# Optimization experiments

Measured on AMD Instinct MI355X. Metric: run time of the kernel, lower is better.

## Reference

```python
import jax, jax.numpy as jnp
import numpy as np

B, T_ENC, T_OUT = 64, 1024, 1000
N_MELS, ENC_D, DEC_H, ATTN_D = 80, 256, 256, 256


def setup_inputs() -> dict:
    key = jax.random.key(0)
    ks = jax.random.split(key, 24)

    def p(k, shape, scale=0.05):
        return jax.random.normal(k, shape, dtype=jnp.float32) * scale

    lengths = jax.random.randint(ks[0], (B,), T_ENC // 2, T_ENC + 1)
    enc_mask = (jnp.arange(T_ENC)[None, :] < lengths[:, None]).astype(jnp.float32)
    return {
        "enc_outputs": jax.random.normal(ks[1], (B, T_ENC, ENC_D), dtype=jnp.float32),
        "target_mel": jax.random.normal(ks[2], (B, T_OUT, N_MELS), dtype=jnp.float32),
        # attention params
        "W_enc": p(ks[3], (ATTN_D, ENC_D)), "b_enc": jnp.zeros((ATTN_D,), jnp.float32),
        "W_dec": p(ks[4], (ATTN_D, DEC_H)), "b_dec": jnp.zeros((ATTN_D,), jnp.float32),
        "v_w": p(ks[5], (1, ATTN_D)), "v_b": jnp.zeros((1,), jnp.float32),
        # prenet
        "pre_W1": p(ks[6], (DEC_H, N_MELS)), "pre_b1": jnp.zeros((DEC_H,), jnp.float32),
        "pre_W2": p(ks[7], (DEC_H, DEC_H)), "pre_b2": jnp.zeros((DEC_H,), jnp.float32),
        # LSTMCell (PyTorch gate order i, f, g, o)
        "W_ih": p(ks[8], (4 * DEC_H, DEC_H + ENC_D)), "W_hh": p(ks[9], (4 * DEC_H, DEC_H)),
        "b_ih": jnp.zeros((4 * DEC_H,), jnp.float32), "b_hh": jnp.zeros((4 * DEC_H,), jnp.float32),
        # output heads
        "mel_W": p(ks[10], (N_MELS, DEC_H + ENC_D)), "mel_b": jnp.zeros((N_MELS,), jnp.float32),
        "stop_W": p(ks[11], (1, DEC_H + ENC_D)), "stop_b": jnp.zeros((1,), jnp.float32),
        "enc_mask": enc_mask,
    }


def reference(enc_outputs, target_mel, W_enc, b_enc, W_dec, b_dec, v_w, v_b,
              pre_W1, pre_b1, pre_W2, pre_b2, W_ih, W_hh, b_ih, b_hh,
              mel_W, mel_b, stop_W, stop_b, enc_mask):
    Bsz = enc_outputs.shape[0]
    H = W_hh.shape[1]
    NEG = jnp.float32(-1e9)
    # precompute encoder projection once, as the original does
    attn_enc = jnp.einsum('bte,ae->bta', enc_outputs, W_enc) + b_enc  # (B, T_enc, A)
    # teacher forcing: input at step t is target_mel[t-1], zeros at t=0
    prev_inputs = jnp.concatenate(
        [jnp.zeros_like(target_mel[:, :1]), target_mel[:, :-1]], axis=1)
    xs = jnp.swapaxes(prev_inputs, 0, 1)  # (T_out, B, n_mels)

    def step(carry, prev):
        h, c = carry
        attn_dec = h @ W_dec.T + b_dec                                  # (B, A)
        energy = jnp.tanh(attn_enc + attn_dec[:, None, :]) @ v_w[0] + v_b[0]  # (B, T_enc)
        energy = jnp.where(enc_mask == 0, NEG, energy)
        attn = jax.nn.softmax(energy, axis=-1)
        context = jnp.einsum('bt,btd->bd', attn, enc_outputs)           # (B, enc_d)
        pre = jax.nn.relu(prev @ pre_W1.T + pre_b1)                     # dropout = identity (eval)
        pre = jax.nn.relu(pre @ pre_W2.T + pre_b2)
        x = jnp.concatenate([pre, context], axis=1)
        gates = x @ W_ih.T + b_ih + h @ W_hh.T + b_hh                   # (B, 4H)
        i, f, g, o = jnp.split(gates, 4, axis=1)
        c_new = jax.nn.sigmoid(f) * c + jax.nn.sigmoid(i) * jnp.tanh(g)
        h_new = jax.nn.sigmoid(o) * jnp.tanh(c_new)
        comb = jnp.concatenate([h_new, context], axis=1)
        mel = comb @ mel_W.T + mel_b
        stop = (comb @ stop_W.T + stop_b)[:, 0]
        return (h_new, c_new), (mel, stop)

    h0 = jnp.zeros((Bsz, H), dtype=enc_outputs.dtype)
    _, (mels, stops) = jax.lax.scan(step, (h0, h0), xs)
    return jnp.swapaxes(mels, 0, 1), jnp.swapaxes(stops, 0, 1)
```

## Files before the change

kernel.cpp:

```cpp
#include <hip/hip_runtime.h>
#include <hip/hip_bf16.h>

#define NMEL 80

__device__ __forceinline__ float bf2f(unsigned short u) {
  unsigned v = ((unsigned)u) << 16; float f; __builtin_memcpy(&f, &v, 4); return f;
}
__device__ __forceinline__ unsigned short f2bf_u(float f) {
  __hip_bfloat16 h = __float2bfloat16(f); unsigned short u; __builtin_memcpy(&u, &h, 2); return u;
}
__device__ __forceinline__ float agload(const float* p) {
  return __hip_atomic_load(p, __ATOMIC_RELAXED, __HIP_MEMORY_SCOPE_AGENT);
}
__device__ __forceinline__ void agstore(float* p, float v) {
  __hip_atomic_store(p, v, __ATOMIC_RELAXED, __HIP_MEMORY_SCOPE_AGENT);
}

constexpr size_t OFF_ATTNT = 0;
constexpr size_t SZ_ATTNT = (size_t)64 * 256 * 1024 * 4;
constexpr size_t OFF_PRE2 = OFF_ATTNT + SZ_ATTNT;
constexpr size_t SZ_PRE2 = (size_t)64000 * 256 * 2;
constexpr size_t OFF_WIC4 = OFF_PRE2 + SZ_PRE2;
constexpr size_t SZ_W4 = (size_t)4 * 64 * 256 * 4 * 4;
constexpr size_t OFF_WPRE4 = OFF_WIC4 + SZ_W4;
constexpr size_t OFF_WHH4 = OFF_WPRE4 + SZ_W4;
constexpr size_t OFF_WDECT = OFF_WHH4 + SZ_W4;
constexpr size_t SZ_WDECT = (size_t)4 * 64 * 256 * 4;
constexpr size_t OFF_MELT = OFF_WDECT + SZ_WDECT;
constexpr size_t SZ_MELT = (size_t)4 * 128 * 80 * 4;
constexpr size_t OFF_STOPT = OFF_MELT + SZ_MELT;
constexpr size_t SZ_STOPT = (size_t)4 * 128 * 4;
constexpr size_t OFF_BIASG = OFF_STOPT + SZ_STOPT;
constexpr size_t SZ_BIASG = (size_t)4 * 256 * 4;
constexpr size_t OFF_EXCH = (OFF_BIASG + SZ_BIASG + 255) & ~(size_t)255;
constexpr size_t EXF_DEC = 0;
constexpr size_t EXN_DEC = (size_t)2 * 64 * 4 * 256;
constexpr size_t EXF_GH = EXF_DEC + EXN_DEC;
constexpr size_t EXN_GH = (size_t)2 * 64 * 4 * 1024;
constexpr size_t EXF_CTX = EXF_GH + EXN_GH;
constexpr size_t EXN_CTX = (size_t)64 * 4 * 256;
constexpr size_t EXF_S = EXF_CTX + EXN_CTX;
constexpr size_t EXN_S = 64 * 16;
constexpr size_t EXF_CTR = EXF_S + EXN_S;
constexpr size_t EXN_CTR = 64 * 16;
constexpr size_t EXCH_FLOATS = EXF_CTR + EXN_CTR;
constexpr size_t SZ_EXCH = EXCH_FLOATS * 4;
constexpr size_t WS_NEED = OFF_EXCH + SZ_EXCH;

__global__ __launch_bounds__(256) void prep_weights(
    const float* __restrict__ W_ih, const float* __restrict__ W_hh,
    const float* __restrict__ W_dec, const float* __restrict__ mel_W,
    const float* __restrict__ stop_W, const float* __restrict__ b_ih,
    const float* __restrict__ b_hh,
    float* __restrict__ Wic4, float* __restrict__ Wpre4, float* __restrict__ Whh4,
    float* __restrict__ WdecT, float* __restrict__ MelT, float* __restrict__ StopT,
    float* __restrict__ biasG) {
  int idx = blockIdx.x * 256 + threadIdx.x;
  if (idx < 262144) {
    int q = idx & 3, j = (idx >> 2) & 255, c4 = (idx >> 10) & 63, s = idx >> 16;
    int row = (j >> 6) * 256 + s * 64 + (j & 63);
    Wic4[idx] = W_ih[(size_t)row * 512 + 256 + c4 * 4 + q];
    Wpre4[idx] = W_ih[(size_t)row * 512 + c4 * 4 + q];
    Whh4[idx] = W_hh[(size_t)(j * 4 + q) * 256 + s * 64 + c4];
  } else if (idx < 262144 + 65536) {
    int k = idx - 262144;
    int a = k & 255, hh = (k >> 8) & 63, s = k >> 14;
    WdecT[k] = W_dec[(size_t)a * 256 + s * 64 + hh];
  } else if (idx < 262144 + 65536 + 40960) {
    int k = idx - (262144 + 65536);
    int m = k % 80, r = k / 80;
    int cc = r & 127, s = r >> 7;
    int col = (cc < 64) ? (s * 64 + cc) : (256 + s * 64 + (cc - 64));
    MelT[k] = mel_W[(size_t)m * 512 + col];
  } else if (idx < 262144 + 65536 + 40960 + 512) {
    int k = idx - (262144 + 65536 + 40960);
    int cc = k & 127, s = k >> 7;
    int col = (cc < 64) ? (s * 64 + cc) : (256 + s * 64 + (cc - 64));
    StopT[k] = stop_W[col];
  } else if (idx < 262144 + 65536 + 40960 + 512 + 1024) {
    int k = idx - (262144 + 65536 + 40960 + 512);
    int j = k & 255, s = k >> 8;
    int row = (j >> 6) * 256 + s * 64 + (j & 63);
    biasG[k] = b_ih[row] + b_hh[row];
  }
}

__global__ __launch_bounds__(256) void attn_gemm(const float* __restrict__ enc,
                                                 const float* __restrict__ W_enc,
                                                 const float* __restrict__ b_enc,
                                                 float* __restrict__ attnT) {
  __shared__ unsigned short Alds[64 * 260];
  const int tid = threadIdx.x;
  const int row0 = blockIdx.x * 64;
  const int wv = tid >> 6, lane = tid & 63, nb = wv * 64;
  for (int idx = tid; idx < 64 * 256; idx += 256) {
    int r = idx >> 8, k = idx & 255;
    Alds[r * 260 + k] = f2bf_u(enc[(size_t)(row0 + r) * 256 + k]);
  }
  __syncthreads();
  float acc[64];
#pragma unroll
  for (int n = 0; n < 64; ++n) acc[n] = b_enc[nb + n];
  for (int k8 = 0; k8 < 256; k8 += 8) {
    ushort4 ua = *(const ushort4*)&Alds[lane * 260 + k8];
    ushort4 ub = *(const ushort4*)&Alds[lane * 260 + k8 + 4];
    float a0 = bf2f(ua.x), a1 = bf2f(ua.y), a2 = bf2f(ua.z), a3 = bf2f(ua.w);
    float a4 = bf2f(ub.x), a5 = bf2f(ub.y), a6 = bf2f(ub.z), a7 = bf2f(ub.w);
#pragma unroll
    for (int n = 0; n < 64; ++n) {
      const float4* wp = (const float4*)(W_enc + (size_t)(nb + n) * 256 + k8);
      float4 w0 = wp[0], w1 = wp[1];
      acc[n] = fmaf(a0, w0.x, acc[n]); acc[n] = fmaf(a1, w0.y, acc[n]);
      acc[n] = fmaf(a2, w0.z, acc[n]); acc[n] = fmaf(a3, w0.w, acc[n]);
      acc[n] = fmaf(a4, w1.x, acc[n]); acc[n] = fmaf(a5, w1.y, acc[n]);
      acc[n] = fmaf(a6, w1.z, acc[n]); acc[n] = fmaf(a7, w1.w, acc[n]);
    }
  }
  const float CE = 2.8853900817779268f;
  const int b = row0 >> 10;
  const int te = (row0 & 1023) + lane;
#pragma unroll
  for (int n = 0; n < 64; ++n) {
    int a = nb + n;
    attnT[(((size_t)b) << 18) + (((size_t)(a >> 2)) << 12) + (((size_t)te) << 2) + (a & 3)] =
        acc[n] * CE;
  }
}

__global__ __launch_bounds__(256) void prenet_fused(const float* __restrict__ tmel,
                                                    const float* __restrict__ W1,
                                                    const float* __restrict__ b1,
                                                    const float* __restrict__ W2,
                                                    const float* __restrict__ b2,
                                                    unsigned short* __restrict__ pre2) {
  __shared__ unsigned short Alds[64 * 260];
  const int tid = threadIdx.x;
  const int row0 = blockIdx.x * 64;
  const int wv = tid >> 6, lane = tid & 63, nb = wv * 64;
  for (int idx = tid; idx < 64 * 80; idx += 256) {
    int r = idx / 80, k = idx - r * 80;
    int R = row0 + r;
    float v = (R % 1000 != 0) ? tmel[(size_t)(R - 1) * NMEL + k] : 0.f;
    Alds[r * 260 + k] = f2bf_u(v);
  }
  __syncthreads();
  float acc[64];
#pragma unroll
  for (int n = 0; n < 64; ++n) acc[n] = b1[nb + n];
  for (int k8 = 0; k8 < 80; k8 += 8) {
    ushort4 ua = *(const ushort4*)&Alds[lane * 260 + k8];
    ushort4 ub = *(const ushort4*)&Alds[lane * 260 + k8 + 4];
    float a0 = bf2f(ua.x), a1 = bf2f(ua.y), a2 = bf2f(ua.z), a3 = bf2f(ua.w);
    float a4 = bf2f(ub.x), a5 = bf2f(ub.y), a6 = bf2f(ub.z), a7 = bf2f(ub.w);
#pragma unroll
    for (int n = 0; n < 64; ++n) {
      const float4* wp = (const float4*)(W1 + (size_t)(nb + n) * 80 + k8);
      float4 w0 = wp[0], w1 = wp[1];
      acc[n] = fmaf(a0, w0.x, acc[n]); acc[n] = fmaf(a1, w0.y, acc[n]);
      acc[n] = fmaf(a2, w0.z, acc[n]); acc[n] = fmaf(a3, w0.w, acc[n]);
      acc[n] = fmaf(a4, w1.x, acc[n]); acc[n] = fmaf(a5, w1.y, acc[n]);
      acc[n] = fmaf(a6, w1.z, acc[n]); acc[n] = fmaf(a7, w1.w, acc[n]);
    }
  }
  __syncthreads();
#pragma unroll
  for (int n = 0; n < 64; ++n) Alds[lane * 260 + nb + n] = f2bf_u(fmaxf(acc[n], 0.f));
  __syncthreads();
#pragma unroll
  for (int n = 0; n < 64; ++n) acc[n] = b2[nb + n];
  for (int k8 = 0; k8 < 256; k8 += 8) {
    ushort4 ua = *(const ushort4*)&Alds[lane * 260 + k8];
    ushort4 ub = *(const ushort4*)&Alds[lane * 260 + k8 + 4];
    float a0 = bf2f(ua.x), a1 = bf2f(ua.y), a2 = bf2f(ua.z), a3 = bf2f(ua.w);
    float a4 = bf2f(ub.x), a5 = bf2f(ub.y), a6 = bf2f(ub.z), a7 = bf2f(ub.w);
#pragma unroll
    for (int n = 0; n < 64; ++n) {
      const float4* wp = (const float4*)(W2 + (size_t)(nb + n) * 256 + k8);
      float4 w0 = wp[0], w1 = wp[1];
      acc[n] = fmaf(a0, w0.x, acc[n]); acc[n] = fmaf(a1, w0.y, acc[n]);
      acc[n] = fmaf(a2, w0.z, acc[n]); acc[n] = fmaf(a3, w0.w, acc[n]);
      acc[n] = fmaf(a4, w1.x, acc[n]); acc[n] = fmaf(a5, w1.y, acc[n]);
      acc[n] = fmaf(a6, w1.z, acc[n]); acc[n] = fmaf(a7, w1.w, acc[n]);
    }
  }
  __syncthreads();
#pragma unroll
  for (int n = 0; n < 64; ++n) Alds[lane * 260 + nb + n] = f2bf_u(fmaxf(acc[n], 0.f));
  __syncthreads();
  for (int idx = tid; idx < 64 * 128; idx += 256) {
    int r = idx >> 7, k2 = (idx & 127) * 2;
    unsigned pair = (unsigned)Alds[r * 260 + k2] | ((unsigned)Alds[r * 260 + k2 + 1] << 16);
    *(unsigned*)(pre2 + (size_t)(row0 + r) * 256 + k2) = pair;
  }
}

__global__ __launch_bounds__(256) void decoder_loop(
    const float* __restrict__ attnT, const float* __restrict__ enc,
    const unsigned short* __restrict__ pre2,
    const float* __restrict__ Wic4, const float* __restrict__ Wpre4,
    const float* __restrict__ Whh4, const float* __restrict__ WdecT,
    const float* __restrict__ MelT, const float* __restrict__ StopT,
    const float* __restrict__ biasG,
    float* exch, unsigned* ctr,
    const float* __restrict__ b_dec, const float* __restrict__ v_w,
    const float* __restrict__ v_b, const float* __restrict__ enc_mask,
    const float* __restrict__ mel_b, const float* __restrict__ stop_b,
    float* out) {
  __shared__ float dec_lds[256], v2_lds[256], p_lds[256], ctx_lds[256], gates_lds[256];
  __shared__ float pre_lds[256];
  __shared__ float ctxp_lds[1024];
  __shared__ float c_lds[64], h_lds[64];
  __shared__ float red_lds[8];
  __shared__ float stop_lds[128];
  __shared__ float sv_lds;

  const int tid = threadIdx.x;
  const int wg = blockIdx.x;
  const int b = wg & 63, s = wg >> 6;
  const int lane = tid & 63, wid = tid >> 6;
  const float CE = 2.8853900817779268f;
  const float L2E = 1.4426950408889634f;

  if (tid < 64) c_lds[tid] = 0.f;
  v2_lds[tid] = -2.f * v_w[tid];
  {
    float sp = v_w[tid];
    for (int m = 32; m; m >>= 1) sp += __shfl_xor(sp, m);
    if (lane == 0) red_lds[wid] = sp;
  }
  __syncthreads();
  if (tid == 0) sv_lds = red_lds[0] + red_lds[1] + red_lds[2] + red_lds[3];
  __syncthreads();
  const float Sv = sv_lds;
  const float vb = v_b[0];
  const int te = s * 256 + tid;
  const float maskv = enc_mask[b * 1024 + te];
  const float bdec_r = b_dec[tid];
  const float biasg_r = biasG[s * 256 + tid];
  const float* attn_me4 = attnT + (((size_t)b) << 18) + (((size_t)te) << 2);
  const unsigned short* pre2_b = pre2 + (size_t)b * 1000 * 256;

  float* decP = exch + EXF_DEC;
  float* ghP = exch + EXF_GH;
  float* ctxP = exch + EXF_CTX;
  float* sP = exch + EXF_S;
  unsigned* ctrb = ctr + b * 16;
  unsigned epoch = 0;

  for (int it = 0; it < 1000; ++it) {
    const int par = it & 1;
    float prefv = bf2f(pre2_b[(size_t)it * 256 + tid]);
    {
      const float* dp = decP + ((size_t)(par * 64 + b) * 4) * 256 + tid;
      float d = bdec_r + agload(dp) + agload(dp + 256) + agload(dp + 512) + agload(dp + 768);
      dec_lds[tid] = d * CE;
    }
    __syncthreads();
    float acc = Sv;
#pragma unroll 8
    for (int a4 = 0; a4 < 64; ++a4) {
      float4 t4 = *(const float4*)(attn_me4 + (((size_t)a4) << 12));
      float4 d4 = *(const float4*)&dec_lds[a4 * 4];
      float4 v4 = *(const float4*)&v2_lds[a4 * 4];
      acc = fmaf(v4.x, __builtin_amdgcn_rcpf(1.f + __builtin_amdgcn_exp2f(t4.x + d4.x)), acc);
      acc = fmaf(v4.y, __builtin_amdgcn_rcpf(1.f + __builtin_amdgcn_exp2f(t4.y + d4.y)), acc);
      acc = fmaf(v4.z, __builtin_amdgcn_rcpf(1.f + __builtin_amdgcn_exp2f(t4.z + d4.z)), acc);
      acc = fmaf(v4.w, __builtin_amdgcn_rcpf(1.f + __builtin_amdgcn_exp2f(t4.w + d4.w)), acc);
    }
    float e = acc + vb;
    float p = (maskv != 0.f) ? __builtin_amdgcn_exp2f(e * L2E) : 0.f;
    p_lds[tid] = p;
    {
      float sp = p;
      for (int m = 32; m; m >>= 1) sp += __shfl_xor(sp, m);
      if (lane == 0) red_lds[wid] = sp;
    }
    __syncthreads();
    {
      int d0 = lane * 4;
      const float* ep = enc + ((size_t)(b * 1024 + s * 256 + wid * 64)) * 256 + d0;
      float c0 = 0, c1 = 0, c2 = 0, c3 = 0;
#pragma unroll 4
      for (int tt = 0; tt < 64; ++tt) {
        float pv = p_lds[wid * 64 + tt];
        float4 ev = *(const float4*)(ep + ((size_t)tt) * 256);
        c0 = fmaf(pv, ev.x, c0);
        c1 = fmaf(pv, ev.y, c1);
        c2 = fmaf(pv, ev.z, c2);
        c3 = fmaf(pv, ev.w, c3);
      }
      ctxp_lds[wid * 256 + d0 + 0] = c0;
      ctxp_lds[wid * 256 + d0 + 1] = c1;
      ctxp_lds[wid * 256 + d0 + 2] = c2;
      ctxp_lds[wid * 256 + d0 + 3] = c3;
    }
    __syncthreads();
    {
      float cp = ctxp_lds[tid] + ctxp_lds[256 + tid] + ctxp_lds[512 + tid] + ctxp_lds[768 + tid];
      agstore(ctxP + ((size_t)b * 4 + s) * 256 + tid, cp);
      if (tid == 0) agstore(sP + b * 16 + s, red_lds[0] + red_lds[1] + red_lds[2] + red_lds[3]);
    }
    pre_lds[tid] = prefv;
    __threadfence();
    __syncthreads();
    if (tid == 0) {
      ++epoch;
      __hip_atomic_fetch_add(ctrb, 1u, __ATOMIC_RELEASE, __HIP_MEMORY_SCOPE_AGENT);
      while (__hip_atomic_load(ctrb, __ATOMIC_ACQUIRE, __HIP_MEMORY_SCOPE_AGENT) < 4u * epoch)
        __builtin_amdgcn_s_sleep(1);
    }
    __syncthreads();
    __threadfence();
    {
      float Ssum = agload(sP + b * 16 + 0) + agload(sP + b * 16 + 1) +
                   agload(sP + b * 16 + 2) + agload(sP + b * 16 + 3);
      float rS = 1.f / Ssum;
      const float* cp = ctxP + (size_t)b * 4 * 256 + tid;
      ctx_lds[tid] = (agload(cp) + agload(cp + 256) + agload(cp + 512) + agload(cp + 768)) * rS;
    }
    __syncthreads();
    {
      float g = biasg_r;
      const float* gp = ghP + ((size_t)(par * 64 + b) * 4) * 1024 + (wid * 256 + s * 64 + lane);
      g += agload(gp) + agload(gp + 1024) + agload(gp + 2048) + agload(gp + 3072);
      const float* wp = Wic4 + (size_t)s * 65536 + tid * 4;
      const float* wq = Wpre4 + (size_t)s * 65536 + tid * 4;
#pragma unroll 8
      for (int c4 = 0; c4 < 64; ++c4) {
        float4 wv1 = *(const float4*)(wp + (size_t)c4 * 1024);
        float4 cx = *(const float4*)&ctx_lds[c4 * 4];
        g = fmaf(wv1.x, cx.x, g); g = fmaf(wv1.y, cx.y, g);
        g = fmaf(wv1.z, cx.z, g); g = fmaf(wv1.w, cx.w, g);
        float4 wv2 = *(const float4*)(wq + (size_t)c4 * 1024);
        float4 px = *(const float4*)&pre_lds[c4 * 4];
        g = fmaf(wv2.x, px.x, g); g = fmaf(wv2.y, px.y, g);
        g = fmaf(wv2.z, px.z, g); g = fmaf(wv2.w, px.w, g);
      }
      gates_lds[tid] = g;
    }
    __syncthreads();
    if (tid < 64) {
      float ii = gates_lds[tid], ff = gates_lds[64 + tid];
      float gg = gates_lds[128 + tid], oo = gates_lds[192 + tid];
      float c = c_lds[tid];
      float si = __builtin_amdgcn_rcpf(1.f + __builtin_amdgcn_exp2f(-ii * L2E));
      float sf = __builtin_amdgcn_rcpf(1.f + __builtin_amdgcn_exp2f(-ff * L2E));
      float so = __builtin_amdgcn_rcpf(1.f + __builtin_amdgcn_exp2f(-oo * L2E));
      float tg = 1.f - 2.f * __builtin_amdgcn_rcpf(1.f + __builtin_amdgcn_exp2f(gg * CE));
      float cn = sf * c + si * tg;
      float tc = 1.f - 2.f * __builtin_amdgcn_rcpf(1.f + __builtin_amdgcn_exp2f(cn * CE));
      c_lds[tid] = cn;
      h_lds[tid] = so * tc;
    }
    __syncthreads();
    if (tid >= 128) {
      int cc = tid - 128;
      float xv = (cc < 64) ? h_lds[cc] : ctx_lds[s * 64 + (cc - 64)];
      stop_lds[cc] = StopT[s * 128 + cc] * xv;
    }
    if (tid < 80) {
      float a = (s == 0) ? mel_b[tid] : 0.f;
      const float* mp = MelT + (size_t)s * 10240 + tid;
#pragma unroll 8
      for (int cc = 0; cc < 128; ++cc) {
        float xv = (cc < 64) ? h_lds[cc] : ctx_lds[s * 64 + (cc - 64)];
        a = fmaf(mp[cc * 80], xv, a);
      }
      atomicAdd(&out[(size_t)b * 80000 + it * 80 + tid], a);
    }
    __syncthreads();
    if (tid == 0) {
      float st = (s == 0) ? stop_b[0] : 0.f;
      for (int i = 0; i < 128; ++i) st += stop_lds[i];
      atomicAdd(&out[(size_t)5120000 + b * 1000 + it], st);
    }
    {
      int pn = par ^ 1;
      const float* wd = WdecT + (size_t)s * 16384 + tid;
      float acd = 0.f;
#pragma unroll 8
      for (int hh = 0; hh < 64; ++hh) acd = fmaf(wd[hh * 256], h_lds[hh], acd);
      agstore(decP + ((size_t)(pn * 64 + b) * 4 + s) * 256 + tid, acd);

      const float* wh = Whh4 + (size_t)s * 65536 + tid * 4;
      float g0 = 0, g1 = 0, g2 = 0, g3 = 0;
#pragma unroll 8
      for (int hh = 0; hh < 64; ++hh) {
        float4 wvv = *(const float4*)(wh + (size_t)hh * 1024);
        float hv = h_lds[hh];
        g0 = fmaf(wvv.x, hv, g0);
        g1 = fmaf(wvv.y, hv, g1);
        g2 = fmaf(wvv.z, hv, g2);
        g3 = fmaf(wvv.w, hv, g3);
      }
      float* gq = ghP + ((size_t)(pn * 64 + b) * 4 + s) * 1024 + tid * 4;
      agstore(gq + 0, g0);
      agstore(gq + 1, g1);
      agstore(gq + 2, g2);
      agstore(gq + 3, g3);
    }
    __threadfence();
    __syncthreads();
    if (tid == 0) {
      ++epoch;
      __hip_atomic_fetch_add(ctrb, 1u, __ATOMIC_RELEASE, __HIP_MEMORY_SCOPE_AGENT);
      while (__hip_atomic_load(ctrb, __ATOMIC_ACQUIRE, __HIP_MEMORY_SCOPE_AGENT) < 4u * epoch)
        __builtin_amdgcn_s_sleep(1);
    }
    __syncthreads();
    __threadfence();
  }
}

extern "C" void kernel_launch(void* const* d_in, const int* in_sizes, int n_in,
                              void* d_out, int out_size, void* d_ws, size_t ws_size,
                              hipStream_t stream) {
  const float* enc = (const float*)d_in[0];
  const float* tmel = (const float*)d_in[1];
  const float* W_enc = (const float*)d_in[2];
  const float* b_enc = (const float*)d_in[3];
  const float* W_dec = (const float*)d_in[4];
  const float* b_dec = (const float*)d_in[5];
  const float* v_w = (const float*)d_in[6];
  const float* v_b = (const float*)d_in[7];
  const float* pW1 = (const float*)d_in[8];
  const float* pb1 = (const float*)d_in[9];
  const float* pW2 = (const float*)d_in[10];
  const float* pb2 = (const float*)d_in[11];
  const float* W_ih = (const float*)d_in[12];
  const float* W_hh = (const float*)d_in[13];
  const float* b_ih = (const float*)d_in[14];
  const float* b_hh = (const float*)d_in[15];
  const float* mel_W = (const float*)d_in[16];
  const float* mel_b = (const float*)d_in[17];
  const float* stop_W = (const float*)d_in[18];
  const float* stop_b = (const float*)d_in[19];
  const float* emask = (const float*)d_in[20];

  if (ws_size < WS_NEED) return;

  char* ws = (char*)d_ws;
  float* attnT = (float*)(ws + OFF_ATTNT);
  unsigned short* pre2 = (unsigned short*)(ws + OFF_PRE2);
  float* Wic4 = (float*)(ws + OFF_WIC4);
  float* Wpre4 = (float*)(ws + OFF_WPRE4);
  float* Whh4 = (float*)(ws + OFF_WHH4);
  float* WdecT = (float*)(ws + OFF_WDECT);
  float* MelT = (float*)(ws + OFF_MELT);
  float* StopT = (float*)(ws + OFF_STOPT);
  float* biasG = (float*)(ws + OFF_BIASG);
  float* exch = (float*)(ws + OFF_EXCH);
  unsigned* ctr = (unsigned*)(exch + EXF_CTR);

  hipMemsetAsync(exch, 0, SZ_EXCH, stream);
  hipMemsetAsync(d_out, 0, (size_t)out_size * 4, stream);

  prep_weights<<<1446, 256, 0, stream>>>(W_ih, W_hh, W_dec, mel_W, stop_W, b_ih, b_hh,
                                         Wic4, Wpre4, Whh4, WdecT, MelT, StopT, biasG);
  attn_gemm<<<1024, 256, 0, stream>>>(enc, W_enc, b_enc, attnT);
  prenet_fused<<<1000, 256, 0, stream>>>(tmel, pW1, pb1, pW2, pb2, pre2);
  decoder_loop<<<256, 256, 0, stream>>>(attnT, enc, pre2, Wic4, Wpre4, Whh4, WdecT, MelT,
                                        StopT, biasG, exch, ctr, b_dec, v_w, v_b, emask,
                                        mel_b, stop_b, (float*)d_out);
}
```

Measured before the change: 169.8 ms.

## Widen decoder blocks to 1024 threads and store attention projection in bf16

The persistent decoder loop moves from 256 to 1024 threads per block, splitting each per-step dot product (energy, context, gates, W_hh and W_dec projections) into four chunks reduced through LDS. This shortens the serial per-thread work on each recurrent step. The precomputed encoder attention projection is now stored as bf16 in an 8-wide interleaved layout, halving its per-step read traffic. The weight layouts are reordered to match the new thread mapping. The cost is extra LDS reductions and barriers per step, plus some precision loss in the attention energies.

```diff
diff --git a/kernel.cpp b/kernel.cpp
--- a/kernel.cpp
+++ b/kernel.cpp
@@ -15,18 +15,29 @@
 __device__ __forceinline__ void agstore(float* p, float v) {
   __hip_atomic_store(p, v, __ATOMIC_RELAXED, __HIP_MEMORY_SCOPE_AGENT);
 }
-
-constexpr size_t OFF_ATTNT = 0;
-constexpr size_t SZ_ATTNT = (size_t)64 * 256 * 1024 * 4;
-constexpr size_t OFF_PRE2 = OFF_ATTNT + SZ_ATTNT;
+__device__ __forceinline__ void unpk(unsigned u, float& lo, float& hi) {
+  unsigned l = u << 16, h = u & 0xffff0000u;
+  __builtin_memcpy(&lo, &l, 4); __builtin_memcpy(&hi, &h, 4);
+}
+struct F8 { float a0, a1, a2, a3, a4, a5, a6, a7; };
+__device__ __forceinline__ F8 unpk8(uint4 u) {
+  F8 r;
+  unpk(u.x, r.a0, r.a1); unpk(u.y, r.a2, r.a3);
+  unpk(u.z, r.a4, r.a5); unpk(u.w, r.a6, r.a7);
+  return r;
+}
+
+constexpr size_t OFF_ATTN8 = 0;
+constexpr size_t SZ_ATTN8 = (size_t)64 * 256 * 1024 * 2;
+constexpr size_t OFF_PRE2 = OFF_ATTN8 + SZ_ATTN8;
 constexpr size_t SZ_PRE2 = (size_t)64000 * 256 * 2;
-constexpr size_t OFF_WIC4 = OFF_PRE2 + SZ_PRE2;
-constexpr size_t SZ_W4 = (size_t)4 * 64 * 256 * 4 * 4;
-constexpr size_t OFF_WPRE4 = OFF_WIC4 + SZ_W4;
-constexpr size_t OFF_WHH4 = OFF_WPRE4 + SZ_W4;
-constexpr size_t OFF_WDECT = OFF_WHH4 + SZ_W4;
-constexpr size_t SZ_WDECT = (size_t)4 * 64 * 256 * 4;
-constexpr size_t OFF_MELT = OFF_WDECT + SZ_WDECT;
+constexpr size_t OFF_WG4 = OFF_PRE2 + SZ_PRE2;
+constexpr size_t SZ_W4 = (size_t)262144 * 4;
+constexpr size_t OFF_WP4 = OFF_WG4 + SZ_W4;
+constexpr size_t OFF_WHH4 = OFF_WP4 + SZ_W4;
+constexpr size_t OFF_WDEC4 = OFF_WHH4 + SZ_W4;
+constexpr size_t SZ_WDEC4 = (size_t)65536 * 4;
+constexpr size_t OFF_MELT = OFF_WDEC4 + SZ_WDEC4;
 constexpr size_t SZ_MELT = (size_t)4 * 128 * 80 * 4;
 constexpr size_t OFF_STOPT = OFF_MELT + SZ_MELT;
 constexpr size_t SZ_STOPT = (size_t)4 * 128 * 4;
@@ -52,35 +63,38 @@
     const float* __restrict__ W_dec, const float* __restrict__ mel_W,
     const float* __restrict__ stop_W, const float* __restrict__ b_ih,
     const float* __restrict__ b_hh,
-    float* __restrict__ Wic4, float* __restrict__ Wpre4, float* __restrict__ Whh4,
-    float* __restrict__ WdecT, float* __restrict__ MelT, float* __restrict__ StopT,
-    float* __restrict__ biasG) {
+    float* __restrict__ Wg4, float* __restrict__ Wp4,
+    float* __restrict__ Whh4, float* __restrict__ Wdec4,
+    float* __restrict__ MelT, float* __restrict__ StopT, float* __restrict__ biasG) {
   int idx = blockIdx.x * 256 + threadIdx.x;
   if (idx < 262144) {
-    int q = idx & 3, j = (idx >> 2) & 255, c4 = (idx >> 10) & 63, s = idx >> 16;
-    int row = (j >> 6) * 256 + s * 64 + (j & 63);
-    Wic4[idx] = W_ih[(size_t)row * 512 + 256 + c4 * 4 + q];
-    Wpre4[idx] = W_ih[(size_t)row * 512 + c4 * 4 + q];
-    Whh4[idx] = W_hh[(size_t)(j * 4 + q) * 256 + s * 64 + c4];
-  } else if (idx < 262144 + 65536) {
-    int k = idx - 262144;
-    int a = k & 255, hh = (k >> 8) & 63, s = k >> 14;
-    WdecT[k] = W_dec[(size_t)a * 256 + s * 64 + hh];
-  } else if (idx < 262144 + 65536 + 40960) {
-    int k = idx - (262144 + 65536);
+    int q = idx & 3, r = (idx >> 2) & 255, kq = (idx >> 10) & 63, s = idx >> 16;
+    int grow = ((r >> 6) << 8) + s * 64 + (r & 63);
+    Wg4[idx] = W_ih[(size_t)grow * 512 + 256 + kq * 4 + q];
+    Wp4[idx] = W_ih[(size_t)grow * 512 + kq * 4 + q];
+  } else if (idx < 524288) {
+    int i = idx - 262144;
+    int q = i & 3, rr = (i >> 2) & 1023, hq = (i >> 12) & 15, s = i >> 16;
+    Whh4[i] = W_hh[(size_t)rr * 256 + s * 64 + hq * 4 + q];
+  } else if (idx < 589824) {
+    int i = idx - 524288;
+    int q = i & 3, a = (i >> 2) & 255, hq = (i >> 10) & 15, s = (i >> 14) & 3;
+    Wdec4[i] = W_dec[(size_t)a * 256 + s * 64 + hq * 4 + q];
+  } else if (idx < 589824 + 40960) {
+    int k = idx - 589824;
     int m = k % 80, r = k / 80;
     int cc = r & 127, s = r >> 7;
     int col = (cc < 64) ? (s * 64 + cc) : (256 + s * 64 + (cc - 64));
     MelT[k] = mel_W[(size_t)m * 512 + col];
-  } else if (idx < 262144 + 65536 + 40960 + 512) {
-    int k = idx - (262144 + 65536 + 40960);
+  } else if (idx < 589824 + 40960 + 512) {
+    int k = idx - (589824 + 40960);
     int cc = k & 127, s = k >> 7;
     int col = (cc < 64) ? (s * 64 + cc) : (256 + s * 64 + (cc - 64));
     StopT[k] = stop_W[col];
-  } else if (idx < 262144 + 65536 + 40960 + 512 + 1024) {
-    int k = idx - (262144 + 65536 + 40960 + 512);
+  } else if (idx < 589824 + 40960 + 512 + 1024) {
+    int k = idx - (589824 + 40960 + 512);
     int j = k & 255, s = k >> 8;
-    int row = (j >> 6) * 256 + s * 64 + (j & 63);
+    int row = ((j >> 6) << 8) + s * 64 + (j & 63);
     biasG[k] = b_ih[row] + b_hh[row];
   }
 }
@@ -88,7 +102,7 @@
 __global__ __launch_bounds__(256) void attn_gemm(const float* __restrict__ enc,
                                                  const float* __restrict__ W_enc,
                                                  const float* __restrict__ b_enc,
-                                                 float* __restrict__ attnT) {
+                                                 unsigned short* __restrict__ attn8) {
   __shared__ unsigned short Alds[64 * 260];
   const int tid = threadIdx.x;
   const int row0 = blockIdx.x * 64;
@@ -120,10 +134,12 @@
   const int b = row0 >> 10;
   const int te = (row0 & 1023) + lane;
 #pragma unroll
-  for (int n = 0; n < 64; ++n) {
-    int a = nb + n;
-    attnT[(((size_t)b) << 18) + (((size_t)(a >> 2)) << 12) + (((size_t)te) << 2) + (a & 3)] =
-        acc[n] * CE;
+  for (int n = 0; n < 64; n += 2) {
+    int a0i = nb + n;
+    unsigned pair = (unsigned)f2bf_u(acc[n] * CE) | ((unsigned)f2bf_u(acc[n + 1] * CE) << 16);
+    size_t elem = (((size_t)b) << 18) + (((size_t)(a0i >> 3)) << 13) + (((size_t)te) << 3) +
+                  (a0i & 7);
+    *(unsigned*)(attn8 + elem) = pair;
   }
 }
 
@@ -194,11 +210,11 @@
   }
 }
 
-__global__ __launch_bounds__(256) void decoder_loop(
-    const float* __restrict__ attnT, const float* __restrict__ enc,
+__global__ __launch_bounds__(1024) void decoder_loop(
+    const unsigned short* __restrict__ attn8, const float* __restrict__ enc,
     const unsigned short* __restrict__ pre2,
-    const float* __restrict__ Wic4, const float* __restrict__ Wpre4,
-    const float* __restrict__ Whh4, const float* __restrict__ WdecT,
+    const float* __restrict__ Wg4, const float* __restrict__ Wp4,
+    const float* __restrict__ Whh4, const float* __restrict__ Wdec4,
     const float* __restrict__ MelT, const float* __restrict__ StopT,
     const float* __restrict__ biasG,
     float* exch, unsigned* ctr,
@@ -206,39 +222,55 @@
     const float* __restrict__ v_b, const float* __restrict__ enc_mask,
     const float* __restrict__ mel_b, const float* __restrict__ stop_b,
     float* out) {
-  __shared__ float dec_lds[256], v2_lds[256], p_lds[256], ctx_lds[256], gates_lds[256];
-  __shared__ float pre_lds[256];
-  __shared__ float ctxp_lds[1024];
+  __shared__ __align__(16) float dec_lds[256];
+  __shared__ __align__(16) float v2_lds[256];
+  __shared__ __align__(16) float p_lds[256];
+  __shared__ __align__(16) float ctx_lds[256];
+  __shared__ __align__(16) float pre_lds[256];
+  __shared__ float gates_lds[256];
+  __shared__ __align__(16) float tmp_lds[1024];
+  __shared__ __align__(16) float ctxp_lds[32 * 256];
+  __shared__ float gpart_lds[1024];
+  __shared__ float dpart_lds[1024];
   __shared__ float c_lds[64], h_lds[64];
-  __shared__ float red_lds[8];
+  __shared__ float red_lds[16];
   __shared__ float stop_lds[128];
   __shared__ float sv_lds;
 
   const int tid = threadIdx.x;
-  const int wg = blockIdx.x;
-  const int b = wg & 63, s = wg >> 6;
+  const int b = blockIdx.x & 63, s = blockIdx.x >> 6;
+  const int t8 = tid & 255;
+  const int chunk = tid >> 8;
   const int lane = tid & 63, wid = tid >> 6;
   const float CE = 2.8853900817779268f;
   const float L2E = 1.4426950408889634f;
 
-  if (tid < 64) c_lds[tid] = 0.f;
-  v2_lds[tid] = -2.f * v_w[tid];
-  {
-    float sp = v_w[tid];
-    for (int m = 32; m; m >>= 1) sp += __shfl_xor(sp, m);
-    if (lane == 0) red_lds[wid] = sp;
-  }
-  __syncthreads();
-  if (tid == 0) sv_lds = red_lds[0] + red_lds[1] + red_lds[2] + red_lds[3];
+  if (tid < 256) {
+    v2_lds[tid] = -2.f * v_w[tid];
+    if (tid < 64) c_lds[tid] = 0.f;
+  }
+  if (tid == 0) {
+    float sv = 0.f;
+    for (int k = 0; k < 256; ++k) sv += v_w[k];
+    sv_lds = sv;
+  }
   __syncthreads();
   const float Sv = sv_lds;
   const float vb = v_b[0];
-  const int te = s * 256 + tid;
-  const float maskv = enc_mask[b * 1024 + te];
-  const float bdec_r = b_dec[tid];
-  const float biasg_r = biasG[s * 256 + tid];
-  const float* attn_me4 = attnT + (((size_t)b) << 18) + (((size_t)te) << 2);
-  const unsigned short* pre2_b = pre2 + (size_t)b * 1000 * 256;
+  const float maskv = (tid < 256) ? enc_mask[b * 1024 + s * 256 + tid] : 0.f;
+  const float bdec_r = (tid < 256) ? b_dec[tid] : 0.f;
+  const float biasg_r = (tid < 256) ? biasG[s * 256 + tid] : 0.f;
+
+  const uint4* ap = (const uint4*)attn8 + (((size_t)b) << 15) +
+                    (((size_t)(chunk * 8)) << 10) + (s * 256 + t8);
+  const int tg = tid >> 5, dl = tid & 31;
+  const float* ep = enc + ((size_t)(b * 1024 + s * 256 + tg * 8)) * 256 + dl * 8;
+  const float4* wg4 = (const float4*)Wg4 + ((size_t)(s * 64 + chunk * 16)) * 256 + t8;
+  const float4* wp4 = (const float4*)Wp4 + ((size_t)(s * 64 + chunk * 16)) * 256 + t8;
+  const int grow = ((t8 >> 6) << 8) + s * 64 + (t8 & 63);
+  const float4* wh4 = (const float4*)Whh4 + ((size_t)s) * 16384 + tid;
+  const float4* wd4 = (const float4*)Wdec4 + ((size_t)(s * 16 + chunk * 4)) * 256 + t8;
+  const unsigned short* pre2_b = pre2 + (size_t)b * 256000;
 
   float* decP = exch + EXF_DEC;
   float* ghP = exch + EXF_GH;
@@ -249,58 +281,76 @@
 
   for (int it = 0; it < 1000; ++it) {
     const int par = it & 1;
-    float prefv = bf2f(pre2_b[(size_t)it * 256 + tid]);
-    {
-      const float* dp = decP + ((size_t)(par * 64 + b) * 4) * 256 + tid;
-      float d = bdec_r + agload(dp) + agload(dp + 256) + agload(dp + 512) + agload(dp + 768);
-      dec_lds[tid] = d * CE;
-    }
-    __syncthreads();
-    float acc = Sv;
-#pragma unroll 8
-    for (int a4 = 0; a4 < 64; ++a4) {
-      float4 t4 = *(const float4*)(attn_me4 + (((size_t)a4) << 12));
-      float4 d4 = *(const float4*)&dec_lds[a4 * 4];
-      float4 v4 = *(const float4*)&v2_lds[a4 * 4];
-      acc = fmaf(v4.x, __builtin_amdgcn_rcpf(1.f + __builtin_amdgcn_exp2f(t4.x + d4.x)), acc);
-      acc = fmaf(v4.y, __builtin_amdgcn_rcpf(1.f + __builtin_amdgcn_exp2f(t4.y + d4.y)), acc);
-      acc = fmaf(v4.z, __builtin_amdgcn_rcpf(1.f + __builtin_amdgcn_exp2f(t4.z + d4.z)), acc);
-      acc = fmaf(v4.w, __builtin_amdgcn_rcpf(1.f + __builtin_amdgcn_exp2f(t4.w + d4.w)), acc);
-    }
-    float e = acc + vb;
-    float p = (maskv != 0.f) ? __builtin_amdgcn_exp2f(e * L2E) : 0.f;
-    p_lds[tid] = p;
-    {
+    const int pn = par ^ 1;
+    float prefv = (tid < 256) ? bf2f(pre2_b[it * 256 + tid]) : 0.f;
+    tmp_lds[tid] = agload(decP + ((size_t)(par * 64 + b)) * 1024 + tid);
+    __syncthreads();
+    if (tid < 256)
+      dec_lds[tid] = (bdec_r + tmp_lds[tid] + tmp_lds[256 + tid] + tmp_lds[512 + tid] +
+                      tmp_lds[768 + tid]) * CE;
+    __syncthreads();
+    float acc = 0.f;
+#pragma unroll
+    for (int i = 0; i < 8; ++i) {
+      uint4 u = ap[(size_t)i << 10];
+      int ab = chunk * 64 + i * 8;
+      float4 d0 = *(const float4*)&dec_lds[ab];
+      float4 d1 = *(const float4*)&dec_lds[ab + 4];
+      float4 v0 = *(const float4*)&v2_lds[ab];
+      float4 v1 = *(const float4*)&v2_lds[ab + 4];
+      F8 t = unpk8(u);
+      acc = fmaf(v0.x, __builtin_amdgcn_rcpf(1.f + __builtin_amdgcn_exp2f(t.a0 + d0.x)), acc);
+      acc = fmaf(v0.y, __builtin_amdgcn_rcpf(1.f + __builtin_amdgcn_exp2f(t.a1 + d0.y)), acc);
+      acc = fmaf(v0.z, __builtin_amdgcn_rcpf(1.f + __builtin_amdgcn_exp2f(t.a2 + d0.z)), acc);
+      acc = fmaf(v0.w, __builtin_amdgcn_rcpf(1.f + __builtin_amdgcn_exp2f(t.a3 + d0.w)), acc);
+      acc = fmaf(v1.x, __builtin_amdgcn_rcpf(1.f + __builtin_amdgcn_exp2f(t.a4 + d1.x)), acc);
+      acc = fmaf(v1.y, __builtin_amdgcn_rcpf(1.f + __builtin_amdgcn_exp2f(t.a5 + d1.y)), acc);
+      acc = fmaf(v1.z, __builtin_amdgcn_rcpf(1.f + __builtin_amdgcn_exp2f(t.a6 + d1.z)), acc);
+      acc = fmaf(v1.w, __builtin_amdgcn_rcpf(1.f + __builtin_amdgcn_exp2f(t.a7 + d1.w)), acc);
+    }
+    tmp_lds[tid] = acc;
+    __syncthreads();
+    if (tid < 256) {
+      float e = Sv + vb + tmp_lds[t8] + tmp_lds[256 + t8] + tmp_lds[512 + t8] + tmp_lds[768 + t8];
+      float p = (maskv != 0.f) ? __builtin_amdgcn_exp2f(e * L2E) : 0.f;
+      p_lds[t8] = p;
       float sp = p;
       for (int m = 32; m; m >>= 1) sp += __shfl_xor(sp, m);
       if (lane == 0) red_lds[wid] = sp;
     }
     __syncthreads();
     {
-      int d0 = lane * 4;
-      const float* ep = enc + ((size_t)(b * 1024 + s * 256 + wid * 64)) * 256 + d0;
-      float c0 = 0, c1 = 0, c2 = 0, c3 = 0;
-#pragma unroll 4
-      for (int tt = 0; tt < 64; ++tt) {
-        float pv = p_lds[wid * 64 + tt];
-        float4 ev = *(const float4*)(ep + ((size_t)tt) * 256);
-        c0 = fmaf(pv, ev.x, c0);
-        c1 = fmaf(pv, ev.y, c1);
-        c2 = fmaf(pv, ev.z, c2);
-        c3 = fmaf(pv, ev.w, c3);
+      float c0 = 0, c1 = 0, c2 = 0, c3 = 0, c4 = 0, c5 = 0, c6 = 0, c7 = 0;
+#pragma unroll
+      for (int j = 0; j < 8; ++j) {
+        const float4* er = (const float4*)(ep + (size_t)j * 256);
+        float4 e0 = er[0], e1 = er[1];
+        float pv = p_lds[tg * 8 + j];
+        c0 = fmaf(pv, e0.x, c0); c1 = fmaf(pv, e0.y, c1);
+        c2 = fmaf(pv, e0.z, c2); c3 = fmaf(pv, e0.w, c3);
+        c4 = fmaf(pv, e1.x, c4); c5 = fmaf(pv, e1.y, c5);
+        c6 = fmaf(pv, e1.z, c6); c7 = fmaf(pv, e1.w, c7);
       }
-      ctxp_lds[wid * 256 + d0 + 0] = c0;
-      ctxp_lds[wid * 256 + d0 + 1] = c1;
-      ctxp_lds[wid * 256 + d0 + 2] = c2;
-      ctxp_lds[wid * 256 + d0 + 3] = c3;
+      float* cb = &ctxp_lds[tg * 256 + dl * 8];
+      cb[0] = c0; cb[1] = c1; cb[2] = c2; cb[3] = c3;
+      cb[4] = c4; cb[5] = c5; cb[6] = c6; cb[7] = c7;
     }
     __syncthreads();
     {
-      float cp = ctxp_lds[tid] + ctxp_lds[256 + tid] + ctxp_lds[512 + tid] + ctxp_lds[768 + tid];
-      agstore(ctxP + ((size_t)b * 4 + s) * 256 + tid, cp);
-      if (tid == 0) agstore(sP + b * 16 + s, red_lds[0] + red_lds[1] + red_lds[2] + red_lds[3]);
-    }
-    pre_lds[tid] = prefv;
+      float scc = 0.f;
+#pragma unroll
+      for (int j = 0; j < 8; ++j) scc += ctxp_lds[(chunk * 8 + j) * 256 + t8];
+      if (tid < 256) pre_lds[tid] = prefv;
+      __syncthreads();
+      tmp_lds[tid] = scc;
+      __syncthreads();
+    }
+    if (tid < 256) {
+      float cp = tmp_lds[t8] + tmp_lds[256 + t8] + tmp_lds[512 + t8] + tmp_lds[768 + t8];
+      agstore(ctxP + ((size_t)b * 4 + s) * 256 + t8, cp);
+    }
+    if (tid == 0)
+      agstore(sP + b * 16 + s, red_lds[0] + red_lds[1] + red_lds[2] + red_lds[3]);
     __threadfence();
     __syncthreads();
     if (tid == 0) {
@@ -310,34 +360,34 @@
         __builtin_amdgcn_s_sleep(1);
     }
     __syncthreads();
-    __threadfence();
+    tmp_lds[tid] = agload(ctxP + ((size_t)b * 4 + chunk) * 256 + t8);
+    if (tid < 4) red_lds[8 + tid] = agload(sP + b * 16 + tid);
+    __syncthreads();
+    if (tid < 256) {
+      float rS = 1.f / (red_lds[8] + red_lds[9] + red_lds[10] + red_lds[11]);
+      ctx_lds[t8] = (tmp_lds[t8] + tmp_lds[256 + t8] + tmp_lds[512 + t8] + tmp_lds[768 + t8]) * rS;
+    }
+    __syncthreads();
     {
-      float Ssum = agload(sP + b * 16 + 0) + agload(sP + b * 16 + 1) +
-                   agload(sP + b * 16 + 2) + agload(sP + b * 16 + 3);
-      float rS = 1.f / Ssum;
-      const float* cp = ctxP + (size_t)b * 4 * 256 + tid;
-      ctx_lds[tid] = (agload(cp) + agload(cp + 256) + agload(cp + 512) + agload(cp + 768)) * rS;
-    }
-    __syncthreads();
-    {
-      float g = biasg_r;
-      const float* gp = ghP + ((size_t)(par * 64 + b) * 4) * 1024 + (wid * 256 + s * 64 + lane);
-      g += agload(gp) + agload(gp + 1024) + agload(gp + 2048) + agload(gp + 3072);
-      const float* wp = Wic4 + (size_t)s * 65536 + tid * 4;
-      const float* wq = Wpre4 + (size_t)s * 65536 + tid * 4;
-#pragma unroll 8
-      for (int c4 = 0; c4 < 64; ++c4) {
-        float4 wv1 = *(const float4*)(wp + (size_t)c4 * 1024);
-        float4 cx = *(const float4*)&ctx_lds[c4 * 4];
-        g = fmaf(wv1.x, cx.x, g); g = fmaf(wv1.y, cx.y, g);
-        g = fmaf(wv1.z, cx.z, g); g = fmaf(wv1.w, cx.w, g);
-        float4 wv2 = *(const float4*)(wq + (size_t)c4 * 1024);
-        float4 px = *(const float4*)&pre_lds[c4 * 4];
-        g = fmaf(wv2.x, px.x, g); g = fmaf(wv2.y, px.y, g);
-        g = fmaf(wv2.z, px.z, g); g = fmaf(wv2.w, px.w, g);
+      float g = agload(ghP + ((size_t)(par * 64 + b)) * 4096 + chunk * 1024 + grow);
+#pragma unroll
+      for (int i = 0; i < 16; ++i) {
+        float4 w = wg4[(size_t)i << 8];
+        float4 q = wp4[(size_t)i << 8];
+        int kb = chunk * 64 + i * 4;
+        float4 x = *(const float4*)&ctx_lds[kb];
+        float4 y = *(const float4*)&pre_lds[kb];
+        g = fmaf(w.x, x.x, g); g = fmaf(w.y, x.y, g);
+        g = fmaf(w.z, x.z, g); g = fmaf(w.w, x.w, g);
+        g = fmaf(q.x, y.x, g); g = fmaf(q.y, y.y, g);
+        g = fmaf(q.z, y.z, g); g = fmaf(q.w, y.w, g);
       }
-      gates_lds[tid] = g;
-    }
+      gpart_lds[tid] = g;
+    }
+    __syncthreads();
+    if (tid < 256)
+      gates_lds[t8] = biasg_r + gpart_lds[t8] + gpart_lds[256 + t8] + gpart_lds[512 + t8] +
+                      gpart_lds[768 + t8];
     __syncthreads();
     if (tid < 64) {
       float ii = gates_lds[tid], ff = gates_lds[64 + tid];
@@ -346,14 +396,14 @@
       float si = __builtin_amdgcn_rcpf(1.f + __builtin_amdgcn_exp2f(-ii * L2E));
       float sf = __builtin_amdgcn_rcpf(1.f + __builtin_amdgcn_exp2f(-ff * L2E));
       float so = __builtin_amdgcn_rcpf(1.f + __builtin_amdgcn_exp2f(-oo * L2E));
-      float tg = 1.f - 2.f * __builtin_amdgcn_rcpf(1.f + __builtin_amdgcn_exp2f(gg * CE));
-      float cn = sf * c + si * tg;
+      float tg2 = 1.f - 2.f * __builtin_amdgcn_rcpf(1.f + __builtin_amdgcn_exp2f(gg * CE));
+      float cn = sf * c + si * tg2;
       float tc = 1.f - 2.f * __builtin_amdgcn_rcpf(1.f + __builtin_amdgcn_exp2f(cn * CE));
       c_lds[tid] = cn;
       h_lds[tid] = so * tc;
     }
     __syncthreads();
-    if (tid >= 128) {
+    if (tid >= 128 && tid < 256) {
       int cc = tid - 128;
       float xv = (cc < 64) ? h_lds[cc] : ctx_lds[s * 64 + (cc - 64)];
       stop_lds[cc] = StopT[s * 128 + cc] * xv;
@@ -368,36 +418,35 @@
       }
       atomicAdd(&out[(size_t)b * 80000 + it * 80 + tid], a);
     }
-    __syncthreads();
+    {
+      float gd = 0.f;
+#pragma unroll
+      for (int i = 0; i < 4; ++i) {
+        float4 w = wd4[(size_t)i << 8];
+        int hb = chunk * 16 + i * 4;
+        gd = fmaf(w.x, h_lds[hb + 0], gd); gd = fmaf(w.y, h_lds[hb + 1], gd);
+        gd = fmaf(w.z, h_lds[hb + 2], gd); gd = fmaf(w.w, h_lds[hb + 3], gd);
+      }
+      dpart_lds[tid] = gd;
+    }
+    {
+      float gh = 0.f;
+#pragma unroll
+      for (int hq = 0; hq < 16; ++hq) {
+        float4 w = wh4[(size_t)hq << 10];
+        gh = fmaf(w.x, h_lds[hq * 4 + 0], gh); gh = fmaf(w.y, h_lds[hq * 4 + 1], gh);
+        gh = fmaf(w.z, h_lds[hq * 4 + 2], gh); gh = fmaf(w.w, h_lds[hq * 4 + 3], gh);
+      }
+      agstore(ghP + ((size_t)(pn * 64 + b) * 4 + s) * 1024 + tid, gh);
+    }
+    __syncthreads();
+    if (tid < 256)
+      agstore(decP + ((size_t)(pn * 64 + b) * 4 + s) * 256 + t8,
+              dpart_lds[t8] + dpart_lds[256 + t8] + dpart_lds[512 + t8] + dpart_lds[768 + t8]);
     if (tid == 0) {
       float st = (s == 0) ? stop_b[0] : 0.f;
-      for (int i = 0; i < 128; ++i) st += stop_lds[i];
+      for (int i2 = 0; i2 < 128; ++i2) st += stop_lds[i2];
       atomicAdd(&out[(size_t)5120000 + b * 1000 + it], st);
-    }
-    {
-      int pn = par ^ 1;
-      const float* wd = WdecT + (size_t)s * 16384 + tid;
-      float acd = 0.f;
-#pragma unroll 8
-      for (int hh = 0; hh < 64; ++hh) acd = fmaf(wd[hh * 256], h_lds[hh], acd);
-      agstore(decP + ((size_t)(pn * 64 + b) * 4 + s) * 256 + tid, acd);
-
-      const float* wh = Whh4 + (size_t)s * 65536 + tid * 4;
-      float g0 = 0, g1 = 0, g2 = 0, g3 = 0;
-#pragma unroll 8
-      for (int hh = 0; hh < 64; ++hh) {
-        float4 wvv = *(const float4*)(wh + (size_t)hh * 1024);
-        float hv = h_lds[hh];
-        g0 = fmaf(wvv.x, hv, g0);
-        g1 = fmaf(wvv.y, hv, g1);
-        g2 = fmaf(wvv.z, hv, g2);
-        g3 = fmaf(wvv.w, hv, g3);
-      }
-      float* gq = ghP + ((size_t)(pn * 64 + b) * 4 + s) * 1024 + tid * 4;
-      agstore(gq + 0, g0);
-      agstore(gq + 1, g1);
-      agstore(gq + 2, g2);
-      agstore(gq + 3, g3);
     }
     __threadfence();
     __syncthreads();
@@ -408,7 +457,6 @@
         __builtin_amdgcn_s_sleep(1);
     }
     __syncthreads();
-    __threadfence();
   }
 }
 
@@ -440,12 +488,12 @@
   if (ws_size < WS_NEED) return;
 
   char* ws = (char*)d_ws;
-  float* attnT = (float*)(ws + OFF_ATTNT);
+  unsigned short* attn8 = (unsigned short*)(ws + OFF_ATTN8);
   unsigned short* pre2 = (unsigned short*)(ws + OFF_PRE2);
-  float* Wic4 = (float*)(ws + OFF_WIC4);
-  float* Wpre4 = (float*)(ws + OFF_WPRE4);
+  float* Wg4 = (float*)(ws + OFF_WG4);
+  float* Wp4 = (float*)(ws + OFF_WP4);
   float* Whh4 = (float*)(ws + OFF_WHH4);
-  float* WdecT = (float*)(ws + OFF_WDECT);
+  float* Wdec4 = (float*)(ws + OFF_WDEC4);
   float* MelT = (float*)(ws + OFF_MELT);
   float* StopT = (float*)(ws + OFF_STOPT);
   float* biasG = (float*)(ws + OFF_BIASG);
@@ -455,11 +503,11 @@
   hipMemsetAsync(exch, 0, SZ_EXCH, stream);
   hipMemsetAsync(d_out, 0, (size_t)out_size * 4, stream);
 
-  prep_weights<<<1446, 256, 0, stream>>>(W_ih, W_hh, W_dec, mel_W, stop_W, b_ih, b_hh,
-                                         Wic4, Wpre4, Whh4, WdecT, MelT, StopT, biasG);
-  attn_gemm<<<1024, 256, 0, stream>>>(enc, W_enc, b_enc, attnT);
+  prep_weights<<<2470, 256, 0, stream>>>(W_ih, W_hh, W_dec, mel_W, stop_W, b_ih, b_hh,
+                                         Wg4, Wp4, Whh4, Wdec4, MelT, StopT, biasG);
+  attn_gemm<<<1024, 256, 0, stream>>>(enc, W_enc, b_enc, attn8);
   prenet_fused<<<1000, 256, 0, stream>>>(tmel, pW1, pb1, pW2, pb2, pre2);
-  decoder_loop<<<256, 256, 0, stream>>>(attnT, enc, pre2, Wic4, Wpre4, Whh4, WdecT, MelT,
-                                        StopT, biasG, exch, ctr, b_dec, v_w, v_b, emask,
-                                        mel_b, stop_b, (float*)d_out);
-}
+  decoder_loop<<<256, 1024, 0, stream>>>(attn8, enc, pre2, Wg4, Wp4, Whh4, Wdec4,
+                                         MelT, StopT, biasG, exch, ctr, b_dec, v_w, v_b,
+                                         emask, mel_b, stop_b, (float*)d_out);
+}
```

Measured after the change: 275.1 ms. +62.0%, slower.
